# Kernel optimization log

Measured on AMD Instinct MI355X. Metric: run time of the kernel, lower is better.

Reference implementation:

```python
import jax, jax.numpy as jnp
import numpy as np

HID = 256
E = 2 * HID  # 512, attention embed dim
H = 2        # attention heads


def _lin(x, w, b):
    return x @ w.T + b


def setup_inputs() -> dict:
    key = jax.random.key(0)
    ks = jax.random.split(key, 16)
    N, Ng, G = 65536, 4096, 16
    s = 0.02
    def w(k, o, i):
        return jax.random.normal(k, (o, i), jnp.float32) * s
    return {
        "flat_pair_enc": jax.random.normal(ks[0], (N, E), jnp.float32),
        "flat_pair_encA": jax.random.normal(ks[1], (N, E + 2), jnp.float32),
        "attn_in_w": w(ks[2], 3 * E, E), "attn_in_b": jnp.zeros(3 * E, jnp.float32),
        "attn_out_w": w(ks[3], E, E), "attn_out_b": jnp.zeros(E, jnp.float32),
        "phi1_w1": w(ks[4], HID, E + 2), "phi1_b1": jnp.zeros(HID, jnp.float32),
        "phi1_w2": w(ks[5], HID, HID), "phi1_b2": jnp.zeros(HID, jnp.float32),
        "phi1_w3": w(ks[6], HID, HID), "phi1_b3": jnp.zeros(HID, jnp.float32),
        "phi1_w4": w(ks[7], E, HID), "phi1_b4": jnp.zeros(E, jnp.float32),
        "g_w1": w(ks[8], HID, E), "g_b1": jnp.zeros(HID, jnp.float32),
        "g_w2": w(ks[9], HID, HID), "g_b2": jnp.zeros(HID, jnp.float32),
        "g_w3": w(ks[10], HID, HID), "g_b3": jnp.zeros(HID, jnp.float32),
        "g_w4": w(ks[11], 1, HID), "g_b4": jnp.zeros(1, jnp.float32),
        "phi2_w1": w(ks[12], HID, E), "phi2_b1": jnp.zeros(HID, jnp.float32),
        "phi2_w2": w(ks[13], HID, HID), "phi2_b2": jnp.zeros(HID, jnp.float32),
        "phi2_w3": w(ks[14], 2, HID), "phi2_b3": jnp.zeros(2, jnp.float32),
        "num_groups": 4096,
        "group_size": 16,
    }


def reference(flat_pair_enc, flat_pair_encA,
              attn_in_w, attn_in_b, attn_out_w, attn_out_b,
              phi1_w1, phi1_b1, phi1_w2, phi1_b2, phi1_w3, phi1_b3, phi1_w4, phi1_b4,
              g_w1, g_b1, g_w2, g_b2, g_w3, g_b3, g_w4, g_b4,
              phi2_w1, phi2_b1, phi2_w2, phi2_b2, phi2_w3, phi2_b3,
              num_groups, group_size):
    elu = jax.nn.elu
    Ng, G = num_groups, group_size
    # phi1 (note the double ELU after the second Linear, as in the source)
    h = elu(_lin(flat_pair_encA, phi1_w1, phi1_b1))
    h = elu(elu(_lin(h, phi1_w2, phi1_b2)))
    h = elu(_lin(h, phi1_w3, phi1_b3))
    key1 = _lin(h, phi1_w4, phi1_b4)                      # (N, E)
    x = key1.reshape(Ng, G, E)                            # segmented groups
    # per-group MultiheadAttention (torch semantics: packed in_proj, scale 1/sqrt(dh))
    qkv = x @ attn_in_w.T + attn_in_b                     # (Ng, G, 3E)
    q, k, v = jnp.split(qkv, 3, axis=-1)
    dh = E // H
    def heads(t):
        return t.reshape(Ng, G, H, dh).transpose(0, 2, 1, 3)  # (Ng, H, G, dh)
    q, k, v = heads(q), heads(k), heads(v)
    scores = jnp.einsum('nhqd,nhkd->nhqk', q, k) / jnp.sqrt(jnp.float32(dh))
    a = jax.nn.softmax(scores, axis=-1)
    o = jnp.einsum('nhqk,nhkd->nhqd', a, v).transpose(0, 2, 1, 3).reshape(Ng, G, E)
    key1_mean = (o @ attn_out_w.T + attn_out_b).mean(axis=1)  # (Ng, E) — mean over seq
    # g head
    hg = elu(_lin(key1_mean, g_w1, g_b1))
    hg = elu(_lin(hg, g_w2, g_b2))
    hg = elu(_lin(hg, g_w3, g_b3))
    q_jt = _lin(hg, g_w4, g_b4)                           # (Ng, 1)
    # alt values: k2 + kbar1 - key1/|g|  (counts per group == G)
    alt_val = flat_pair_enc.reshape(Ng, G, E) + key1_mean[:, None, :] - x / G
    hp = elu(_lin(alt_val, phi2_w1, phi2_b1))
    hp = elu(_lin(hp, phi2_w2, phi2_b2))
    alt_q = _lin(hp, phi2_w3, phi2_b3)                    # (Ng, G, 2)
    return (q_jt, alt_q)
```

## Files before the change

kernel.cpp:

```cpp
#include <hip/hip_runtime.h>
#include <cstdint>

typedef __bf16 bf16;
typedef __attribute__((ext_vector_type(8))) __bf16 bf16x8;
typedef __attribute__((ext_vector_type(4))) __bf16 bf16x4;
typedef __attribute__((ext_vector_type(4))) float f32x4;
typedef __attribute__((ext_vector_type(2))) float f32x2;

static __device__ __forceinline__ float elu1(float x) {
    return x > 0.f ? x : (__expf(x) - 1.f);
}

static __device__ __forceinline__ void gl_lds16(const void* gp, void* lp) {
    __builtin_amdgcn_global_load_lds(
        (const __attribute__((address_space(1))) void*)(uintptr_t)gp,
        (__attribute__((address_space(3))) void*)(uint32_t)(uintptr_t)lp,
        16, 0, 0);
}

struct CvtArgs {
    const float* src[13];
    int rows[13];
    int scols[13];
    int dcols[13];
    int total;
};

__global__ void cvt_k(CvtArgs a, bf16* __restrict__ dst) {
    int idx = blockIdx.x * 256 + threadIdx.x;
    if (idx >= a.total) return;
    int rem = idx;
#pragma unroll 1
    for (int s = 0; s < 13; ++s) {
        int sz = a.rows[s] * a.dcols[s];
        if (rem < sz) {
            int r = rem / a.dcols[s];
            int c = rem - r * a.dcols[s];
            float v = (c < a.scols[s]) ? a.src[s][(long)r * a.scols[s] + c] : 0.f;
            dst[idx] = (bf16)v;
            return;
        }
        rem -= sz;
    }
}

struct GemmArgs {
    const float* Af;
    const bf16*  Ab;
    long lda;
    const float* enc;
    const float* km;
    const bf16*  key1;
    const bf16*  W;
    long ldw;
    const float* bias;
    bf16*  Cb;
    float* Cf;
    long ldc;
    int nK;
    int klim;
};

enum { AM_F32 = 0, AM_F32U = 1, AM_BF16 = 2, AM_ALT = 3 };
enum { ACT_NONE = 0, ACT_ELU = 1, ACT_ELU2 = 2 };

template <int AMODE, int ACT, bool OUTB>
__global__ __launch_bounds__(256, 2) void gemm_t(GemmArgs g) {
    __shared__ bf16 As[128 * 64];
    __shared__ bf16 Bs[128 * 64];

    const int tid  = threadIdx.x;
    const int wave = tid >> 6;
    const int lane = tid & 63;
    const int ln   = lane & 15;
    const int quad = lane >> 4;

    const long m0 = (long)blockIdx.x * 128;
    const long n0 = (long)blockIdx.y * 128;
    const int  wm = (wave & 1) * 64;
    const int  wn = (wave >> 1) * 64;

    f32x4 acc[4][4] = {};

    for (int ks = 0; ks < g.nK; ++ks) {
        const int k0 = ks * 64;
        __syncthreads();

        if constexpr (AMODE == AM_BF16) {
            const int cbase = wave * 256;
#pragma unroll
            for (int r = 0; r < 4; ++r) {
                const int c = cbase + r * 64 + lane;
                const int m = c >> 3, s = c & 7;
                const int pg = (s - m) & 7;
                gl_lds16(g.Ab + (m0 + m) * g.lda + k0 + pg * 8, &As[c * 8]);
            }
        } else {
#pragma unroll
            for (int r = 0; r < 4; ++r) {
                const int c = r * 256 + tid;
                const int m = c >> 3, s = c & 7;
                const int pg = (s - m) & 7;
                const int kk = k0 + pg * 8;
                bf16x8 t;
                if constexpr (AMODE == AM_F32) {
                    const float* ap = g.Af + (m0 + m) * g.lda + kk;
                    f32x4 p0 = *(const f32x4*)ap;
                    f32x4 p1 = *(const f32x4*)(ap + 4);
                    t[0] = (bf16)p0.x; t[1] = (bf16)p0.y; t[2] = (bf16)p0.z; t[3] = (bf16)p0.w;
                    t[4] = (bf16)p1.x; t[5] = (bf16)p1.y; t[6] = (bf16)p1.z; t[7] = (bf16)p1.w;
                } else if constexpr (AMODE == AM_F32U) {
                    const float* ap = g.Af + (m0 + m) * g.lda;
                    if (kk + 8 <= g.klim) {
#pragma unroll
                        for (int e = 0; e < 8; e += 2) {
                            f32x2 p = *(const f32x2*)(ap + kk + e);
                            t[e] = (bf16)p.x; t[e + 1] = (bf16)p.y;
                        }
                    } else {
#pragma unroll
                        for (int e = 0; e < 8; ++e) {
                            const int col = kk + e;
                            t[e] = (bf16)(col < g.klim ? ap[col] : 0.f);
                        }
                    }
                } else {
                    const long row = m0 + m;
                    const float* ep = g.enc + row * 512 + kk;
                    const float* mp = g.km + (row >> 4) * 512 + kk;
                    const bf16*  xp = g.key1 + row * 512 + kk;
                    f32x4 e0 = *(const f32x4*)ep;
                    f32x4 e1 = *(const f32x4*)(ep + 4);
                    f32x4 q0 = *(const f32x4*)mp;
                    f32x4 q1 = *(const f32x4*)(mp + 4);
                    bf16x8 x8 = *(const bf16x8*)xp;
                    t[0] = (bf16)(e0.x + q0.x - (float)x8[0] * 0.0625f);
                    t[1] = (bf16)(e0.y + q0.y - (float)x8[1] * 0.0625f);
                    t[2] = (bf16)(e0.z + q0.z - (float)x8[2] * 0.0625f);
                    t[3] = (bf16)(e0.w + q0.w - (float)x8[3] * 0.0625f);
                    t[4] = (bf16)(e1.x + q1.x - (float)x8[4] * 0.0625f);
                    t[5] = (bf16)(e1.y + q1.y - (float)x8[5] * 0.0625f);
                    t[6] = (bf16)(e1.z + q1.z - (float)x8[6] * 0.0625f);
                    t[7] = (bf16)(e1.w + q1.w - (float)x8[7] * 0.0625f);
                }
                *(bf16x8*)(&As[m * 64 + s * 8]) = t;
            }
        }

        {
            const int cbase = wave * 256;
#pragma unroll
            for (int r = 0; r < 4; ++r) {
                const int c = cbase + r * 64 + lane;
                const int n = c >> 3, s = c & 7;
                const int pg = (s - n) & 7;
                gl_lds16(g.W + (n0 + n) * g.ldw + k0 + pg * 8, &Bs[c * 8]);
            }
        }
        __syncthreads();

#pragma unroll
        for (int ksub = 0; ksub < 2; ++ksub) {
            bf16x8 av[4], bv[4];
#pragma unroll
            for (int t = 0; t < 4; ++t) {
                const int m = wm + t * 16 + ln;
                const int sa = ((ksub * 4 + quad) + m) & 7;
                av[t] = *(const bf16x8*)(&As[m * 64 + sa * 8]);
                const int n = wn + t * 16 + ln;
                const int sb = ((ksub * 4 + quad) + n) & 7;
                bv[t] = *(const bf16x8*)(&Bs[n * 64 + sb * 8]);
            }
#pragma unroll
            for (int i = 0; i < 4; ++i)
#pragma unroll
                for (int j = 0; j < 4; ++j)
                    acc[i][j] = __builtin_amdgcn_mfma_f32_16x16x32_bf16(
                        av[i], bv[j], acc[i][j], 0, 0, 0);
        }
    }

#pragma unroll
    for (int i = 0; i < 4; ++i) {
        const long rb = m0 + wm + i * 16 + quad * 4;
#pragma unroll
        for (int j = 0; j < 4; ++j) {
            const long n = n0 + wn + j * 16 + ln;
            const float bvs = g.bias[n];
#pragma unroll
            for (int r = 0; r < 4; ++r) {
                float v = acc[i][j][r] + bvs;
                if constexpr (ACT >= ACT_ELU) v = elu1(v);
                if constexpr (ACT == ACT_ELU2) v = elu1(v);
                const long o = (rb + r) * g.ldc + n;
                if constexpr (OUTB) g.Cb[o] = (bf16)v;
                else                g.Cf[o] = v;
            }
        }
    }
}

__global__ __launch_bounds__(256) void attn_k(const bf16* __restrict__ qkv,
                                              bf16* __restrict__ obar,
                                              int ngroups) {
    const int tid = blockIdx.x * 256 + threadIdx.x;
    const int wv = tid >> 6;
    const int g  = wv >> 1;
    const int h  = wv & 1;
    if (g >= ngroups) return;
    const int lane = threadIdx.x & 63;
    const int i  = lane & 15;
    const int jb = (lane >> 4) << 2;

    const bf16* base  = qkv + (long)g * 16 * 1536;
    const bf16* qrow  = base + (long)i * 1536 + h * 256;
    const bf16* kbase = base + 512 + h * 256;

    float s0 = 0.f, s1 = 0.f, s2 = 0.f, s3 = 0.f;
    for (int kk = 0; kk < 256; kk += 8) {
        bf16x8 qv = *(const bf16x8*)(qrow + kk);
        float qf[8];
#pragma unroll
        for (int e = 0; e < 8; ++e) qf[e] = (float)qv[e];
        bf16x8 k0 = *(const bf16x8*)(kbase + (long)(jb + 0) * 1536 + kk);
        bf16x8 k1 = *(const bf16x8*)(kbase + (long)(jb + 1) * 1536 + kk);
        bf16x8 k2 = *(const bf16x8*)(kbase + (long)(jb + 2) * 1536 + kk);
        bf16x8 k3 = *(const bf16x8*)(kbase + (long)(jb + 3) * 1536 + kk);
#pragma unroll
        for (int e = 0; e < 8; ++e) {
            s0 += qf[e] * (float)k0[e];
            s1 += qf[e] * (float)k1[e];
            s2 += qf[e] * (float)k2[e];
            s3 += qf[e] * (float)k3[e];
        }
    }
    const float sc = 1.f / 16.f;
    s0 *= sc; s1 *= sc; s2 *= sc; s3 *= sc;
    float m = fmaxf(fmaxf(s0, s1), fmaxf(s2, s3));
    m = fmaxf(m, __shfl_xor(m, 16));
    m = fmaxf(m, __shfl_xor(m, 32));
    float e0 = __expf(s0 - m), e1 = __expf(s1 - m), e2 = __expf(s2 - m), e3 = __expf(s3 - m);
    float rs = e0 + e1 + e2 + e3;
    rs += __shfl_xor(rs, 16);
    rs += __shfl_xor(rs, 32);
    const float inv = 1.f / (rs * 16.f);
    float cb[4] = {e0 * inv, e1 * inv, e2 * inv, e3 * inv};
#pragma unroll
    for (int msk = 1; msk <= 8; msk <<= 1) {
        cb[0] += __shfl_xor(cb[0], msk);
        cb[1] += __shfl_xor(cb[1], msk);
        cb[2] += __shfl_xor(cb[2], msk);
        cb[3] += __shfl_xor(cb[3], msk);
    }
    float call[16];
#pragma unroll
    for (int j = 0; j < 16; ++j)
        call[j] = __shfl(cb[j & 3], (j >> 2) << 4);

    const int d0 = lane << 2;
    const bf16* vb = base + 1024 + h * 256 + d0;
    float o0 = 0.f, o1 = 0.f, o2 = 0.f, o3 = 0.f;
#pragma unroll
    for (int j = 0; j < 16; ++j) {
        bf16x4 vv = *(const bf16x4*)(vb + (long)j * 1536);
        o0 += call[j] * (float)vv[0];
        o1 += call[j] * (float)vv[1];
        o2 += call[j] * (float)vv[2];
        o3 += call[j] * (float)vv[3];
    }
    bf16x4 ov;
    ov[0] = (bf16)o0; ov[1] = (bf16)o1; ov[2] = (bf16)o2; ov[3] = (bf16)o3;
    *(bf16x4*)(obar + (long)g * 512 + h * 256 + d0) = ov;
}

__global__ void qjt_k(const bf16* __restrict__ hg, const bf16* __restrict__ w,
                      const float* __restrict__ b, float* __restrict__ out) {
    const int m = blockIdx.x * 256 + threadIdx.x;
    const bf16* hp = hg + (long)m * 256;
    float acc = 0.f;
    for (int k = 0; k < 256; k += 8) {
        bf16x8 hv = *(const bf16x8*)(hp + k);
        bf16x8 wv = *(const bf16x8*)(w + k);
#pragma unroll
        for (int e = 0; e < 8; ++e) acc += (float)hv[e] * (float)wv[e];
    }
    out[m] = acc + b[0];
}

__global__ void altq_k(const bf16* __restrict__ hp, const bf16* __restrict__ w,
                       const float* __restrict__ b, float* __restrict__ out) {
    const int m = blockIdx.x * 256 + threadIdx.x;
    const bf16* hr = hp + (long)m * 256;
    float a0 = 0.f, a1 = 0.f;
    for (int k = 0; k < 256; k += 8) {
        bf16x8 hv = *(const bf16x8*)(hr + k);
        bf16x8 w0 = *(const bf16x8*)(w + k);
        bf16x8 w1 = *(const bf16x8*)(w + 256 + k);
#pragma unroll
        for (int e = 0; e < 8; ++e) {
            float hf = (float)hv[e];
            a0 += hf * (float)w0[e];
            a1 += hf * (float)w1[e];
        }
    }
    out[2 * m]     = a0 + b[0];
    out[2 * m + 1] = a1 + b[1];
}

extern "C" void kernel_launch(void* const* d_in, const int* in_sizes, int n_in,
                              void* d_out, int out_size, void* d_ws, size_t ws_size,
                              hipStream_t stream) {
    const float* enc    = (const float*)d_in[0];
    const float* encA   = (const float*)d_in[1];
    const float* w_ain  = (const float*)d_in[2];
    const float* b_ain  = (const float*)d_in[3];
    const float* w_aout = (const float*)d_in[4];
    const float* b_aout = (const float*)d_in[5];
    const float* w_p11  = (const float*)d_in[6];
    const float* b_p11  = (const float*)d_in[7];
    const float* w_p12  = (const float*)d_in[8];
    const float* b_p12  = (const float*)d_in[9];
    const float* w_p13  = (const float*)d_in[10];
    const float* b_p13  = (const float*)d_in[11];
    const float* w_p14  = (const float*)d_in[12];
    const float* b_p14  = (const float*)d_in[13];
    const float* w_g1   = (const float*)d_in[14];
    const float* b_g1   = (const float*)d_in[15];
    const float* w_g2   = (const float*)d_in[16];
    const float* b_g2   = (const float*)d_in[17];
    const float* w_g3   = (const float*)d_in[18];
    const float* b_g3   = (const float*)d_in[19];
    const float* w_g4   = (const float*)d_in[20];
    const float* b_g4   = (const float*)d_in[21];
    const float* w_p21  = (const float*)d_in[22];
    const float* b_p21  = (const float*)d_in[23];
    const float* w_p22  = (const float*)d_in[24];
    const float* b_p22  = (const float*)d_in[25];
    const float* w_p23  = (const float*)d_in[26];
    const float* b_p23  = (const float*)d_in[27];
    float* out = (float*)d_out;

    char* wsc = (char*)d_ws;
    size_t off = 0;
    auto take = [&](size_t bytes) -> char* {
        char* p = wsc + off;
        off += (bytes + 255) & ~(size_t)255;
        return p;
    };

    const long o_ain  = 0;
    const long o_aout = o_ain + 1536L * 512;
    const long o_p11  = o_aout + 512L * 512;
    const long o_p12  = o_p11 + 256L * 576;
    const long o_p13  = o_p12 + 256L * 256;
    const long o_p14  = o_p13 + 256L * 256;
    const long o_g1   = o_p14 + 512L * 256;
    const long o_g2   = o_g1 + 256L * 512;
    const long o_g3   = o_g2 + 256L * 256;
    const long o_g4   = o_g3 + 256L * 256;
    const long o_p21  = o_g4 + 256L;
    const long o_p22  = o_p21 + 256L * 512;
    const long o_p23  = o_p22 + 256L * 256;
    const long wtot   = o_p23 + 2L * 256;

    bf16*  wb  = (bf16*)take((size_t)wtot * 2);
    bf16*  Ha  = (bf16*)take(65536ull * 256 * 2);
    bf16*  Hb  = (bf16*)take(65536ull * 256 * 2);
    bf16*  K1  = (bf16*)take(65536ull * 512 * 2);
    bf16*  OB  = (bf16*)take(4096ull * 512 * 2);
    float* KM  = (float*)take(4096ull * 512 * 4);
    bf16*  HGa = (bf16*)take(4096ull * 256 * 2);
    bf16*  HGb = (bf16*)take(4096ull * 256 * 2);

    int CH = 16;
    if (off + (65536ull / 2) * 1536 * 2 <= ws_size)      CH = 2;
    else if (off + (65536ull / 4) * 1536 * 2 <= ws_size) CH = 4;
    else if (off + (65536ull / 8) * 1536 * 2 <= ws_size) CH = 8;
    bf16* QKV = (bf16*)take((size_t)(65536 / CH) * 1536 * 2);

    CvtArgs ca;
    const float* srcs[13] = {w_ain, w_aout, w_p11, w_p12, w_p13, w_p14,
                             w_g1, w_g2, w_g3, w_g4, w_p21, w_p22, w_p23};
    const int rows_[13]  = {1536, 512, 256, 256, 256, 512, 256, 256, 256, 1, 256, 256, 2};
    const int scols_[13] = {512, 512, 514, 256, 256, 256, 512, 256, 256, 256, 512, 256, 256};
    const int dcols_[13] = {512, 512, 576, 256, 256, 256, 512, 256, 256, 256, 512, 256, 256};
    for (int s = 0; s < 13; ++s) {
        ca.src[s] = srcs[s]; ca.rows[s] = rows_[s];
        ca.scols[s] = scols_[s]; ca.dcols[s] = dcols_[s];
    }
    ca.total = (int)wtot;
    cvt_k<<<dim3((unsigned)((wtot + 255) / 256)), dim3(256), 0, stream>>>(ca, wb);

    GemmArgs ga;

    ga = {}; ga.Af = encA; ga.lda = 514; ga.klim = 514;
    ga.W = wb + o_p11; ga.ldw = 576; ga.bias = b_p11;
    ga.Cb = Ha; ga.ldc = 256; ga.nK = 9;
    gemm_t<AM_F32U, ACT_ELU, true><<<dim3(512, 2), 256, 0, stream>>>(ga);

    ga = {}; ga.Ab = Ha; ga.lda = 256; ga.W = wb + o_p12; ga.ldw = 256;
    ga.bias = b_p12; ga.Cb = Hb; ga.ldc = 256; ga.nK = 4;
    gemm_t<AM_BF16, ACT_ELU2, true><<<dim3(512, 2), 256, 0, stream>>>(ga);

    ga = {}; ga.Ab = Hb; ga.lda = 256; ga.W = wb + o_p13; ga.ldw = 256;
    ga.bias = b_p13; ga.Cb = Ha; ga.ldc = 256; ga.nK = 4;
    gemm_t<AM_BF16, ACT_ELU, true><<<dim3(512, 2), 256, 0, stream>>>(ga);

    ga = {}; ga.Ab = Ha; ga.lda = 256; ga.W = wb + o_p14; ga.ldw = 256;
    ga.bias = b_p14; ga.Cb = K1; ga.ldc = 512; ga.nK = 4;
    gemm_t<AM_BF16, ACT_NONE, true><<<dim3(512, 4), 256, 0, stream>>>(ga);

    const int Mc = 65536 / CH;
    const int gc = 4096 / CH;
    for (int c = 0; c < CH; ++c) {
        ga = {}; ga.Ab = K1 + (long)c * Mc * 512; ga.lda = 512;
        ga.W = wb + o_ain; ga.ldw = 512; ga.bias = b_ain;
        ga.Cb = QKV; ga.ldc = 1536; ga.nK = 8;
        gemm_t<AM_BF16, ACT_NONE, true>
            <<<dim3(Mc / 128, 12), 256, 0, stream>>>(ga);
        attn_k<<<dim3((gc * 2) / 4), 256, 0, stream>>>(QKV, OB + (long)c * gc * 512, gc);
    }

    ga = {}; ga.Ab = OB; ga.lda = 512; ga.W = wb + o_aout; ga.ldw = 512;
    ga.bias = b_aout; ga.Cf = KM; ga.ldc = 512; ga.nK = 8;
    gemm_t<AM_BF16, ACT_NONE, false><<<dim3(32, 4), 256, 0, stream>>>(ga);

    ga = {}; ga.Af = KM; ga.lda = 512; ga.W = wb + o_g1; ga.ldw = 512;
    ga.bias = b_g1; ga.Cb = HGa; ga.ldc = 256; ga.nK = 8;
    gemm_t<AM_F32, ACT_ELU, true><<<dim3(32, 2), 256, 0, stream>>>(ga);

    ga = {}; ga.Ab = HGa; ga.lda = 256; ga.W = wb + o_g2; ga.ldw = 256;
    ga.bias = b_g2; ga.Cb = HGb; ga.ldc = 256; ga.nK = 4;
    gemm_t<AM_BF16, ACT_ELU, true><<<dim3(32, 2), 256, 0, stream>>>(ga);

    ga = {}; ga.Ab = HGb; ga.lda = 256; ga.W = wb + o_g3; ga.ldw = 256;
    ga.bias = b_g3; ga.Cb = HGa; ga.ldc = 256; ga.nK = 4;
    gemm_t<AM_BF16, ACT_ELU, true><<<dim3(32, 2), 256, 0, stream>>>(ga);

    qjt_k<<<dim3(16), 256, 0, stream>>>(HGa, wb + o_g4, b_g4, out);

    ga = {}; ga.enc = enc; ga.km = KM; ga.key1 = K1;
    ga.W = wb + o_p21; ga.ldw = 512; ga.bias = b_p21;
    ga.Cb = Ha; ga.ldc = 256; ga.nK = 8;
    gemm_t<AM_ALT, ACT_ELU, true><<<dim3(512, 2), 256, 0, stream>>>(ga);

    ga = {}; ga.Ab = Ha; ga.lda = 256; ga.W = wb + o_p22; ga.ldw = 256;
    ga.bias = b_p22; ga.Cb = Hb; ga.ldc = 256; ga.nK = 4;
    gemm_t<AM_BF16, ACT_ELU, true><<<dim3(512, 2), 256, 0, stream>>>(ga);

    altq_k<<<dim3(256), 256, 0, stream>>>(Hb, wb + o_p23, b_p23, out + 4096);
}
```

Baseline: 799.2 us.

## Pre-convert padded encA to bf16 and prefetch fp32 A tiles in GEMM

Adds a separate kernel that converts the 514-column fp32 encA input into a zero-padded 576-column bf16 buffer, so the first phi1 GEMM can use the async global-to-LDS bf16 path instead of unaligned fp32 loads. That buffer shares workspace with the QKV chunk buffer. The fp32-input GEMM modes (including the fused alt_val mode) now issue global loads for the next K tile into registers before the MFMA loop, overlapping load latency with compute. The cost is an extra pass over encA (read fp32, write bf16) and higher register pressure in the prefetching modes, which may reduce occupancy.

```diff
diff --git a/kernel.cpp b/kernel.cpp
--- a/kernel.cpp
+++ b/kernel.cpp
@@ -42,6 +42,29 @@
         }
         rem -= sz;
     }
+}
+
+__global__ void cvtA_k(const float* __restrict__ src, bf16* __restrict__ dst) {
+    const int idx = blockIdx.x * 256 + threadIdx.x;
+    const int r = idx / 72;
+    const int c8 = (idx - r * 72) * 8;
+    const float* sp = src + (long)r * 514 + c8;
+    bf16x8 t;
+    if (c8 + 8 <= 514) {
+        f32x2 p0 = *(const f32x2*)(sp + 0);
+        f32x2 p1 = *(const f32x2*)(sp + 2);
+        f32x2 p2 = *(const f32x2*)(sp + 4);
+        f32x2 p3 = *(const f32x2*)(sp + 6);
+        t[0] = (bf16)p0.x; t[1] = (bf16)p0.y; t[2] = (bf16)p1.x; t[3] = (bf16)p1.y;
+        t[4] = (bf16)p2.x; t[5] = (bf16)p2.y; t[6] = (bf16)p3.x; t[7] = (bf16)p3.y;
+    } else {
+#pragma unroll
+        for (int e = 0; e < 8; ++e) {
+            const int col = c8 + e;
+            t[e] = (bf16)(col < 514 ? sp[e] : 0.f);
+        }
+    }
+    *(bf16x8*)(dst + (long)r * 576 + c8) = t;
 }
 
 struct GemmArgs {
@@ -82,6 +105,85 @@
 
     f32x4 acc[4][4] = {};
 
+    int cm[4], cs[4];
+    long ar[4];
+    if constexpr (AMODE != AM_BF16) {
+#pragma unroll
+        for (int r = 0; r < 4; ++r) {
+            const int c = r * 256 + tid;
+            cm[r] = c >> 3;
+            cs[r] = c & 7;
+            ar[r] = m0 + cm[r];
+        }
+    }
+
+    f32x4 pf[4][2];
+    float pu[4][8];
+    f32x4 pe[4][2], pq[4][2];
+    bf16x8 px[4];
+
+    auto loadA = [&](int k0) {
+#pragma unroll
+        for (int r = 0; r < 4; ++r) {
+            const int kk = k0 + (((cs[r] - cm[r]) & 7) << 3);
+            if constexpr (AMODE == AM_F32) {
+                const float* ap = g.Af + ar[r] * g.lda + kk;
+                pf[r][0] = *(const f32x4*)ap;
+                pf[r][1] = *(const f32x4*)(ap + 4);
+            } else if constexpr (AMODE == AM_F32U) {
+                const float* ap = g.Af + ar[r] * g.lda;
+                if (kk + 8 <= g.klim) {
+#pragma unroll
+                    for (int e = 0; e < 8; e += 2) {
+                        f32x2 p = *(const f32x2*)(ap + kk + e);
+                        pu[r][e] = p.x;
+                        pu[r][e + 1] = p.y;
+                    }
+                } else {
+#pragma unroll
+                    for (int e = 0; e < 8; ++e) {
+                        const int col = kk + e;
+                        pu[r][e] = col < g.klim ? ap[col] : 0.f;
+                    }
+                }
+            } else if constexpr (AMODE == AM_ALT) {
+                const float* ep = g.enc + ar[r] * 512 + kk;
+                const float* mp = g.km + (ar[r] >> 4) * 512 + kk;
+                pe[r][0] = *(const f32x4*)ep;
+                pe[r][1] = *(const f32x4*)(ep + 4);
+                pq[r][0] = *(const f32x4*)mp;
+                pq[r][1] = *(const f32x4*)(mp + 4);
+                px[r] = *(const bf16x8*)(g.key1 + ar[r] * 512 + kk);
+            }
+        }
+    };
+
+    auto writeA = [&]() {
+#pragma unroll
+        for (int r = 0; r < 4; ++r) {
+            bf16x8 t;
+            if constexpr (AMODE == AM_F32) {
+#pragma unroll
+                for (int e = 0; e < 4; ++e) {
+                    t[e]     = (bf16)pf[r][0][e];
+                    t[e + 4] = (bf16)pf[r][1][e];
+                }
+            } else if constexpr (AMODE == AM_F32U) {
+#pragma unroll
+                for (int e = 0; e < 8; ++e) t[e] = (bf16)pu[r][e];
+            } else {
+#pragma unroll
+                for (int e = 0; e < 4; ++e) {
+                    t[e]     = (bf16)(pe[r][0][e] + pq[r][0][e] - (float)px[r][e] * 0.0625f);
+                    t[e + 4] = (bf16)(pe[r][1][e] + pq[r][1][e] - (float)px[r][e + 4] * 0.0625f);
+                }
+            }
+            *(bf16x8*)(&As[cm[r] * 64 + cs[r] * 8]) = t;
+        }
+    };
+
+    if constexpr (AMODE != AM_BF16) loadA(0);
+
     for (int ks = 0; ks < g.nK; ++ks) {
         const int k0 = ks * 64;
         __syncthreads();
@@ -96,55 +198,7 @@
                 gl_lds16(g.Ab + (m0 + m) * g.lda + k0 + pg * 8, &As[c * 8]);
             }
         } else {
-#pragma unroll
-            for (int r = 0; r < 4; ++r) {
-                const int c = r * 256 + tid;
-                const int m = c >> 3, s = c & 7;
-                const int pg = (s - m) & 7;
-                const int kk = k0 + pg * 8;
-                bf16x8 t;
-                if constexpr (AMODE == AM_F32) {
-                    const float* ap = g.Af + (m0 + m) * g.lda + kk;
-                    f32x4 p0 = *(const f32x4*)ap;
-                    f32x4 p1 = *(const f32x4*)(ap + 4);
-                    t[0] = (bf16)p0.x; t[1] = (bf16)p0.y; t[2] = (bf16)p0.z; t[3] = (bf16)p0.w;
-                    t[4] = (bf16)p1.x; t[5] = (bf16)p1.y; t[6] = (bf16)p1.z; t[7] = (bf16)p1.w;
-                } else if constexpr (AMODE == AM_F32U) {
-                    const float* ap = g.Af + (m0 + m) * g.lda;
-                    if (kk + 8 <= g.klim) {
-#pragma unroll
-                        for (int e = 0; e < 8; e += 2) {
-                            f32x2 p = *(const f32x2*)(ap + kk + e);
-                            t[e] = (bf16)p.x; t[e + 1] = (bf16)p.y;
-                        }
-                    } else {
-#pragma unroll
-                        for (int e = 0; e < 8; ++e) {
-                            const int col = kk + e;
-                            t[e] = (bf16)(col < g.klim ? ap[col] : 0.f);
-                        }
-                    }
-                } else {
-                    const long row = m0 + m;
-                    const float* ep = g.enc + row * 512 + kk;
-                    const float* mp = g.km + (row >> 4) * 512 + kk;
-                    const bf16*  xp = g.key1 + row * 512 + kk;
-                    f32x4 e0 = *(const f32x4*)ep;
-                    f32x4 e1 = *(const f32x4*)(ep + 4);
-                    f32x4 q0 = *(const f32x4*)mp;
-                    f32x4 q1 = *(const f32x4*)(mp + 4);
-                    bf16x8 x8 = *(const bf16x8*)xp;
-                    t[0] = (bf16)(e0.x + q0.x - (float)x8[0] * 0.0625f);
-                    t[1] = (bf16)(e0.y + q0.y - (float)x8[1] * 0.0625f);
-                    t[2] = (bf16)(e0.z + q0.z - (float)x8[2] * 0.0625f);
-                    t[3] = (bf16)(e0.w + q0.w - (float)x8[3] * 0.0625f);
-                    t[4] = (bf16)(e1.x + q1.x - (float)x8[4] * 0.0625f);
-                    t[5] = (bf16)(e1.y + q1.y - (float)x8[5] * 0.0625f);
-                    t[6] = (bf16)(e1.z + q1.z - (float)x8[6] * 0.0625f);
-                    t[7] = (bf16)(e1.w + q1.w - (float)x8[7] * 0.0625f);
-                }
-                *(bf16x8*)(&As[m * 64 + s * 8]) = t;
-            }
+            writeA();
         }
 
         {
@@ -158,6 +212,10 @@
             }
         }
         __syncthreads();
+
+        if constexpr (AMODE != AM_BF16) {
+            if (ks + 1 < g.nK) loadA(k0 + 64);
+        }
 
 #pragma unroll
         for (int ksub = 0; ksub < 2; ++ksub) {
@@ -372,11 +430,25 @@
     bf16*  HGa = (bf16*)take(4096ull * 256 * 2);
     bf16*  HGb = (bf16*)take(4096ull * 256 * 2);
 
+    const size_t apad_b = 65536ull * 576 * 2;
+    const size_t avail = ws_size > off ? ws_size - off : 0;
+    bool apad_ok = apad_b <= avail;
+    auto qkvb = [](int ch) { return (size_t)(65536 / ch) * 1536 * 2; };
+    auto need = [&](size_t q) {
+        const size_t a = apad_ok ? apad_b : 0;
+        return q > a ? q : a;
+    };
     int CH = 16;
-    if (off + (65536ull / 2) * 1536 * 2 <= ws_size)      CH = 2;
-    else if (off + (65536ull / 4) * 1536 * 2 <= ws_size) CH = 4;
-    else if (off + (65536ull / 8) * 1536 * 2 <= ws_size) CH = 8;
-    bf16* QKV = (bf16*)take((size_t)(65536 / CH) * 1536 * 2);
+    if (need(qkvb(2)) <= avail)      CH = 2;
+    else if (need(qkvb(4)) <= avail) CH = 4;
+    else if (need(qkvb(8)) <= avail) CH = 8;
+    else {
+        CH = 16;
+        if (need(qkvb(16)) > avail) apad_ok = false;
+    }
+    bf16* U = (bf16*)take(need(qkvb(CH)));
+    bf16* Apad = U;
+    bf16* QKV  = U;
 
     CvtArgs ca;
     const float* srcs[13] = {w_ain, w_aout, w_p11, w_p12, w_p13, w_p14,
@@ -390,13 +462,22 @@
     }
     ca.total = (int)wtot;
     cvt_k<<<dim3((unsigned)((wtot + 255) / 256)), dim3(256), 0, stream>>>(ca, wb);
+    if (apad_ok)
+        cvtA_k<<<dim3(18432), dim3(256), 0, stream>>>(encA, Apad);
 
     GemmArgs ga;
 
-    ga = {}; ga.Af = encA; ga.lda = 514; ga.klim = 514;
-    ga.W = wb + o_p11; ga.ldw = 576; ga.bias = b_p11;
-    ga.Cb = Ha; ga.ldc = 256; ga.nK = 9;
-    gemm_t<AM_F32U, ACT_ELU, true><<<dim3(512, 2), 256, 0, stream>>>(ga);
+    if (apad_ok) {
+        ga = {}; ga.Ab = Apad; ga.lda = 576;
+        ga.W = wb + o_p11; ga.ldw = 576; ga.bias = b_p11;
+        ga.Cb = Ha; ga.ldc = 256; ga.nK = 9;
+        gemm_t<AM_BF16, ACT_ELU, true><<<dim3(512, 2), 256, 0, stream>>>(ga);
+    } else {
+        ga = {}; ga.Af = encA; ga.lda = 514; ga.klim = 514;
+        ga.W = wb + o_p11; ga.ldw = 576; ga.bias = b_p11;
+        ga.Cb = Ha; ga.ldc = 256; ga.nK = 9;
+        gemm_t<AM_F32U, ACT_ELU, true><<<dim3(512, 2), 256, 0, stream>>>(ga);
+    }
 
     ga = {}; ga.Ab = Ha; ga.lda = 256; ga.W = wb + o_p12; ga.ldw = 256;
     ga.bias = b_p12; ga.Cb = Hb; ga.ldc = 256; ga.nK = 4;
```

Measured after the change: 787.5 us. No clear change (-1.5%).
